# Performance work log

Measured on AMD Instinct MI355X. Metric: run time of the kernel, lower is better.

Reference implementation:

```python
import math
import jax, jax.numpy as jnp
import numpy as np

C = 128; NH = 8; NL = 4; NP = 4; DFF = 512; L = 3
RH, RW = 80, 240           # Rworld_shape
H, W = RH // 2, RW // 2    # per-level spatial shape after stride-2 downsample


def setup_inputs() -> dict:
    key = jax.random.key(0)
    ks = jax.random.split(key, 25)
    def n(k, shape, s=0.02):
        return jax.random.normal(k, shape, dtype=jnp.float32) * s
    return {
        "x": jax.random.normal(ks[0], (1, NL, C, RH, RW), dtype=jnp.float32),
        "dconv_w": n(ks[1], (C, C, 3, 3)),
        "dconv_b": n(ks[2], (C,)),
        "lvl_emb": n(ks[3], (NL, C), 1.0),
        "W_off": n(ks[4], (L, NH * NL * NP * 2, C)),
        "b_off": n(ks[5], (L, NH * NL * NP * 2), 0.1),
        "W_attn": n(ks[6], (L, NH * NL * NP, C)),
        "b_attn": n(ks[7], (L, NH * NL * NP)),
        "W_val": n(ks[8], (L, C, C)),
        "b_val": n(ks[9], (L, C)),
        "W_out": n(ks[10], (L, C, C)),
        "b_out": n(ks[11], (L, C)),
        "ln1_g": jnp.ones((L, C), jnp.float32),
        "ln1_b": jnp.zeros((L, C), jnp.float32),
        "W_ff1": n(ks[12], (L, DFF, C)),
        "b_ff1": n(ks[13], (L, DFF)),
        "W_ff2": n(ks[14], (L, C, DFF)),
        "b_ff2": n(ks[15], (L, C)),
        "ln2_g": jnp.ones((L, C), jnp.float32),
        "ln2_b": jnp.zeros((L, C), jnp.float32),
        "merge_w": n(ks[16], (C, C * NL, 1, 1)),
        "merge_b": n(ks[17], (C,)),
        "uconv_w": n(ks[18], (C, C, 3, 3)),
        "uconv_b": n(ks[19], (C,)),
    }


def conv2d(x, w, b, stride=1, pad=1):
    y = jax.lax.conv_general_dilated(x, w, (stride, stride), [(pad, pad), (pad, pad)],
                                     dimension_numbers=("NCHW", "OIHW", "NCHW"))
    return y + b[None, :, None, None]


def linear(x, w, b):
    return jnp.einsum("...i,oi->...o", x, w) + b


def layer_norm(x, g, b, eps=1e-5):
    m = jnp.mean(x, -1, keepdims=True)
    v = jnp.var(x, -1, keepdims=True)
    return (x - m) * jax.lax.rsqrt(v + eps) * g + b


def sine_pos_embed(h, w, nf, temperature=10000.0):
    # matches create_pos_embedding with normalize=True, scale=2*pi
    scale = 2.0 * math.pi
    eps = 1e-6
    ye = jnp.arange(1, h + 1, dtype=jnp.float32) / (h + eps) * scale
    xe = jnp.arange(1, w + 1, dtype=jnp.float32) / (w + eps) * scale
    i = jnp.arange(nf, dtype=jnp.float32)
    dim_t = temperature ** (2.0 * jnp.floor(i / 2.0) / nf)
    def enc(e):
        p = e[:, None] / dim_t
        return jnp.stack([jnp.sin(p[:, 0::2]), jnp.cos(p[:, 1::2])], -1).reshape(e.shape[0], nf)
    py, px = enc(ye), enc(xe)
    pos = jnp.concatenate([jnp.broadcast_to(py[:, None, :], (h, w, nf)),
                           jnp.broadcast_to(px[None, :, :], (h, w, nf))], -1)
    return pos  # (h, w, 2*nf) with [pos_y, pos_x] channel order


def ms_deform_attn_core(vmaps, loc, attn):
    # vmaps: (B,NL,NH,H*W,hd); loc: (B,Lq,NH,NL,NP,2) in [0,1] (x,y); attn: (B,Lq,NH,NL,NP)
    # grid_sample(align_corners=False, padding_mode='zeros') bilinear gather
    x = loc[..., 0] * W - 0.5
    y = loc[..., 1] * H - 0.5
    x0 = jnp.floor(x)
    y0 = jnp.floor(y)
    out = jnp.zeros((loc.shape[0], loc.shape[1], NH, vmaps.shape[-1]), loc.dtype)
    for dy in (0, 1):
        for dx in (0, 1):
            xc = x0 + dx
            yc = y0 + dy
            wgt = (1.0 - jnp.abs(x - xc)) * (1.0 - jnp.abs(y - yc))
            valid = (xc >= 0) & (xc < W) & (yc >= 0) & (yc < H)
            xi = jnp.clip(xc, 0, W - 1).astype(jnp.int32)
            yi = jnp.clip(yc, 0, H - 1).astype(jnp.int32)
            idx = (yi * W + xi).transpose(0, 3, 2, 1, 4)  # (B,NL,NH,Lq,NP)
            B_, nl, nh, lq, npt = idx.shape
            g = jnp.take_along_axis(vmaps, idx.reshape(B_, nl, nh, lq * npt, 1),
                                    axis=3).reshape(B_, nl, nh, lq, npt, -1)
            wv = (wgt * jnp.where(valid, 1.0, 0.0) * attn).transpose(0, 3, 2, 1, 4)
            out = out + jnp.einsum("blhqp,blhqpd->bqhd", wv, g)
    return out.reshape(out.shape[0], out.shape[1], -1)  # (B,Lq,NH*hd)


def reference(x, dconv_w, dconv_b, lvl_emb, W_off, b_off, W_attn, b_attn, W_val, b_val,
              W_out, b_out, ln1_g, ln1_b, W_ff1, b_ff1, W_ff2, b_ff2, ln2_g, ln2_b,
              merge_w, merge_b, uconv_w, uconv_b):
    B, N, c, h0, w0 = x.shape
    xs = jax.nn.relu(conv2d(x.reshape(B * N, c, h0, w0), dconv_w, dconv_b, stride=2))
    src = xs.reshape(B, N, c, H, W).transpose(0, 1, 3, 4, 2).reshape(B, N * H * W, c)
    pos = sine_pos_embed(H, W, c // 2).reshape(1, H * W, c) + lvl_emb[:, None, :]
    pos = pos.reshape(1, N * H * W, c)
    # reference points: per-level pixel centers (valid_ratios are all ones)
    ry = (jnp.arange(H, dtype=jnp.float32) + 0.5) / H
    rx = (jnp.arange(W, dtype=jnp.float32) + 0.5) / W
    ref = jnp.stack(jnp.meshgrid(rx, ry, indexing="xy"), -1).reshape(H * W, 2)
    ref = jnp.tile(ref, (N, 1))[None]  # (1, Lq, 2)
    hd = c // NH
    norm = jnp.array([W, H], jnp.float32)
    for i in range(W_off.shape[0]):
        q = src + pos
        value = linear(src, W_val[i], b_val[i]).reshape(B, N, H * W, NH, hd)
        vmaps = value.transpose(0, 1, 3, 2, 4)  # (B,NL,NH,HW,hd)
        off = linear(q, W_off[i], b_off[i]).reshape(B, -1, NH, N, NP, 2)
        aw = jax.nn.softmax(linear(q, W_attn[i], b_attn[i]).reshape(B, -1, NH, N * NP), -1)
        aw = aw.reshape(B, -1, NH, N, NP)
        loc = ref[:, :, None, None, None, :] + off / norm
        attn_out = ms_deform_attn_core(vmaps, loc, aw)
        src = layer_norm(src + linear(attn_out, W_out[i], b_out[i]), ln1_g[i], ln1_b[i])
        ff = linear(jax.nn.relu(linear(src, W_ff1[i], b_ff1[i])), W_ff2[i], b_ff2[i])
        src = layer_norm(src + ff, ln2_g[i], ln2_b[i])
    m = src.reshape(B, N, H, W, c).transpose(0, 1, 4, 2, 3).reshape(B, N * c, H, W)
    m = jax.nn.relu(conv2d(m, merge_w, merge_b, pad=0))
    m = jax.image.resize(m, (B, c, RH, RW), method="bilinear")
    m = jax.nn.relu(conv2d(m, uconv_w, uconv_b))
    return m
```

## Files before the change

kernel.cpp:

```cpp
#include <hip/hip_runtime.h>
#include <math.h>
#include <cstddef>

#define LQ   19200
#define HH   40
#define WW   120
#define HWp  4800
#define CCh  128
#define NHd  8
#define NLv  4
#define NPt  4
#define RHs  80
#define RWs  240

typedef __attribute__((ext_vector_type(8))) short bf16x8;
typedef __attribute__((ext_vector_type(4))) float f32x4;
typedef __attribute__((ext_vector_type(8))) _Float16 h16x8;
typedef __attribute__((address_space(1))) const unsigned int GUI;
typedef __attribute__((address_space(3))) unsigned int LUI;

__device__ inline unsigned short f2bf(float f) {
    unsigned int u = __float_as_uint(f);
    u += 0x7fffu + ((u >> 16) & 1u);
    return (unsigned short)(u >> 16);
}
__device__ inline float bf2f(unsigned int lo16) { return __uint_as_float(lo16 << 16); }

template<bool BIAS_ROW, bool RELU, int OMODE>
__global__ __launch_bounds__(256) void gemm_bf16(
    const unsigned short* __restrict__ A,
    const unsigned short* __restrict__ Bw,
    const float* __restrict__ bias,
    float* __restrict__ OutF, unsigned short* __restrict__ OutB,
    int M, int N, int K)
{
    constexpr int BM = 128, BN = 64, BK = 32;
    __shared__ unsigned short As[2][BM * BK];
    __shared__ unsigned short Bs[2][BN * BK];
    const int bm = blockIdx.y * BM, bn = blockIdx.x * BN;
    const int tid = threadIdx.x;
    const int wid = tid >> 6, lane = tid & 63;
    const int wm = (wid & 1) * 64, wn = (wid >> 1) * 32;
    const int lm = lane & 15, lqd = lane >> 4;

    f32x4 acc[4][2] = {};

    const int arow = lane >> 2;
    const int akc  = (lane & 3) * 8;
    const unsigned short* aG0 = A  + (size_t)(bm + wid * 32 +      arow) * K + akc;
    const unsigned short* aG1 = A  + (size_t)(bm + wid * 32 + 16 + arow) * K + akc;
    const unsigned short* bG  = Bw + (size_t)(bn + wid * 16 +      arow) * K + akc;
    const int aoff = wid * 1024 + lane * 8;
    const int boff = wid * 512 + lane * 8;

    auto stage = [&](int b, int k0) {
        __builtin_amdgcn_global_load_lds((GUI*)(aG0 + k0), (LUI*)(As[b] + aoff), 16, 0, 0);
        __builtin_amdgcn_global_load_lds((GUI*)(aG1 + k0), (LUI*)(As[b] + aoff + 512), 16, 0, 0);
        __builtin_amdgcn_global_load_lds((GUI*)(bG  + k0), (LUI*)(Bs[b] + boff), 16, 0, 0);
    };

    stage(0, 0);
    __syncthreads();
    int buf = 0;
    for (int k0 = 0; k0 < K; k0 += BK, buf ^= 1) {
        if (k0 + BK < K) stage(buf ^ 1, k0 + BK);
        bf16x8 a[4], b[2];
        #pragma unroll
        for (int i = 0; i < 4; i++)
            a[i] = *(const bf16x8*)(As[buf] + (wm + i * 16 + lm) * BK + lqd * 8);
        #pragma unroll
        for (int j = 0; j < 2; j++)
            b[j] = *(const bf16x8*)(Bs[buf] + (wn + j * 16 + lm) * BK + lqd * 8);
        #pragma unroll
        for (int i = 0; i < 4; i++)
            #pragma unroll
            for (int j = 0; j < 2; j++)
                acc[i][j] = __builtin_amdgcn_mfma_f32_16x16x32_bf16(a[i], b[j], acc[i][j], 0, 0, 0);
        __syncthreads();
    }

    #pragma unroll
    for (int i = 0; i < 4; i++) {
        int row0 = bm + wm + i * 16 + lqd * 4;
        #pragma unroll
        for (int j = 0; j < 2; j++) {
            int col = bn + wn + j * 16 + lm;
            float bc = BIAS_ROW ? 0.f : bias[col];
            #pragma unroll
            for (int r = 0; r < 4; r++) {
                int row = row0 + r;
                float v = acc[i][j][r] + (BIAS_ROW ? bias[row] : bc);
                if (RELU) v = fmaxf(v, 0.f);
                size_t o = (size_t)row * N + col;
                if (OMODE == 0) OutF[o] = v;
                else if (OMODE == 1) OutB[o] = f2bf(v);
                else { OutF[o] = v; OutB[o] = f2bf(v); }
            }
        }
    }
}

__global__ __launch_bounds__(256) void gemm_oav(
    const unsigned short* __restrict__ Aq,
    const unsigned short* __restrict__ Asrc,
    const unsigned short* __restrict__ Woa, const float* __restrict__ boa,
    const unsigned short* __restrict__ Wv,  const float* __restrict__ bv,
    _Float16* __restrict__ OutH, _Float16* __restrict__ OutH2,
    unsigned short* __restrict__ OutV)
{
    constexpr int BK = 32, K = 128;
    __shared__ unsigned short As[2][128 * BK];
    __shared__ unsigned short Bs[2][64 * BK];
    const int bx = blockIdx.x;
    const bool isv = bx >= 6;
    const unsigned short* A  = isv ? Asrc : Aq;
    const unsigned short* Bw = isv ? Wv : Woa;
    const float* bias = isv ? bv : boa;
    const int bn = isv ? (bx - 6) * 64 : bx * 64;
    const int bm = blockIdx.y * 128;
    const int tid = threadIdx.x;
    const int wid = tid >> 6, lane = tid & 63;
    const int wm = (wid & 1) * 64, wn = (wid >> 1) * 32;
    const int lm = lane & 15, lqd = lane >> 4;

    f32x4 acc[4][2] = {};

    const int arow = lane >> 2;
    const int akc  = (lane & 3) * 8;
    const unsigned short* aG0 = A  + (size_t)(bm + wid * 32 +      arow) * K + akc;
    const unsigned short* aG1 = A  + (size_t)(bm + wid * 32 + 16 + arow) * K + akc;
    const unsigned short* bG  = Bw + (size_t)(bn + wid * 16 +      arow) * K + akc;
    const int aoff = wid * 1024 + lane * 8;
    const int boff = wid * 512 + lane * 8;

    auto stage = [&](int b, int k0) {
        __builtin_amdgcn_global_load_lds((GUI*)(aG0 + k0), (LUI*)(As[b] + aoff), 16, 0, 0);
        __builtin_amdgcn_global_load_lds((GUI*)(aG1 + k0), (LUI*)(As[b] + aoff + 512), 16, 0, 0);
        __builtin_amdgcn_global_load_lds((GUI*)(bG  + k0), (LUI*)(Bs[b] + boff), 16, 0, 0);
    };

    stage(0, 0);
    __syncthreads();
    int buf = 0;
    for (int k0 = 0; k0 < K; k0 += BK, buf ^= 1) {
        if (k0 + BK < K) stage(buf ^ 1, k0 + BK);
        bf16x8 a[4], b[2];
        #pragma unroll
        for (int i = 0; i < 4; i++)
            a[i] = *(const bf16x8*)(As[buf] + (wm + i * 16 + lm) * BK + lqd * 8);
        #pragma unroll
        for (int j = 0; j < 2; j++)
            b[j] = *(const bf16x8*)(Bs[buf] + (wn + j * 16 + lm) * BK + lqd * 8);
        #pragma unroll
        for (int i = 0; i < 4; i++)
            #pragma unroll
            for (int j = 0; j < 2; j++)
                acc[i][j] = __builtin_amdgcn_mfma_f32_16x16x32_bf16(a[i], b[j], acc[i][j], 0, 0, 0);
        __syncthreads();
    }

    #pragma unroll
    for (int i = 0; i < 4; i++) {
        int row0 = bm + wm + i * 16 + lqd * 4;
        #pragma unroll
        for (int j = 0; j < 2; j++) {
            int col = bn + wn + j * 16 + lm;
            float bc = bias[col];
            if (!isv) {
                if (col < 256) {
                    #pragma unroll
                    for (int r = 0; r < 4; r++)
                        OutH[(size_t)(row0 + r) * 256 + col] = (_Float16)(acc[i][j][r] + bc);
                } else {
                    #pragma unroll
                    for (int r = 0; r < 4; r++) {
                        float v = acc[i][j][r] + bc;
                        float m = v;
                        #pragma unroll
                        for (int msk = 1; msk < 16; msk <<= 1)
                            m = fmaxf(m, __shfl_xor(m, msk));
                        float e = __expf(v - m);
                        float s = e;
                        #pragma unroll
                        for (int msk = 1; msk < 16; msk <<= 1)
                            s += __shfl_xor(s, msk);
                        OutH2[(size_t)(row0 + r) * 128 + (col - 256)] = (_Float16)(e / s);
                    }
                }
            } else {
                #pragma unroll
                for (int r = 0; r < 4; r++) {
                    int row = row0 + r;
                    int plane = (row / HWp) * 8 + (col >> 4);
                    size_t o = ((size_t)plane * HWp + (row % HWp)) * 16 + (col & 15);
                    OutV[o] = f2bf(acc[i][j][r] + bc);
                }
            }
        }
    }
}

template<bool WQ, bool WMERGE>
__global__ __launch_bounds__(256) void attn_ff(
    const unsigned short* __restrict__ attnout, const float* __restrict__ srcF_in,
    const unsigned short* __restrict__ Wout, const float* __restrict__ bout,
    const float* __restrict__ g1, const float* __restrict__ c1,
    const unsigned short* __restrict__ Wff1, const float* __restrict__ bff1,
    const unsigned short* __restrict__ Wff2, const float* __restrict__ bff2,
    const float* __restrict__ g2, const float* __restrict__ c2,
    float* __restrict__ outF, unsigned short* __restrict__ outB,
    const float* __restrict__ pos, unsigned short* __restrict__ qb,
    unsigned short* __restrict__ mergeb)
{
    __shared__ unsigned short fs[32 * 264];
    __shared__ unsigned short y1s[32 * 136];
    __shared__ float red[4][2][32];
    const int bm = blockIdx.x * 32;
    const int tid = threadIdx.x;
    const int wid = tid >> 6, lane = tid & 63;
    const int lm = lane & 15, lqd = lane >> 4;
    const int wn2 = wid * 32;

    float y1r[2][2][4];
    {
        f32x4 accA[2][2] = {};
        for (int k0 = 0; k0 < 128; k0 += 32) {
            int kc = k0 >> 5;
            bf16x8 a[2], b[2];
            #pragma unroll
            for (int i = 0; i < 2; i++)
                a[i] = *(const bf16x8*)(attnout + (size_t)(bm + i * 16 + lm) * 128 + k0 + lqd * 8);
            #pragma unroll
            for (int j = 0; j < 2; j++)
                b[j] = *(const bf16x8*)(Wout + ((size_t)((wid * 2 + j) * 4 + kc) * 64 + lane) * 8);
            #pragma unroll
            for (int i = 0; i < 2; i++)
                #pragma unroll
                for (int j = 0; j < 2; j++)
                    accA[i][j] = __builtin_amdgcn_mfma_f32_16x16x32_bf16(a[i], b[j], accA[i][j], 0, 0, 0);
        }
        #pragma unroll
        for (int i = 0; i < 2; i++)
            #pragma unroll
            for (int j = 0; j < 2; j++) {
                int col = wn2 + j * 16 + lm;
                float bc = bout[col];
                #pragma unroll
                for (int r = 0; r < 4; r++) {
                    int row = bm + i * 16 + lqd * 4 + r;
                    y1r[i][j][r] = accA[i][j][r] + bc + srcF_in[(size_t)row * 128 + col];
                }
            }
    }
    #pragma unroll
    for (int i = 0; i < 2; i++) {
        #pragma unroll
        for (int r = 0; r < 4; r++) {
            float s = y1r[i][0][r] + y1r[i][1][r];
            float q = y1r[i][0][r] * y1r[i][0][r] + y1r[i][1][r] * y1r[i][1][r];
            #pragma unroll
            for (int msk = 1; msk < 16; msk <<= 1) {
                s += __shfl_xor(s, msk);
                q += __shfl_xor(q, msk);
            }
            if (lm == 0) {
                int rl = i * 16 + lqd * 4 + r;
                red[wid][0][rl] = s;
                red[wid][1][rl] = q;
            }
        }
    }
    __syncthreads();
    #pragma unroll
    for (int i = 0; i < 2; i++) {
        float mean[4], inv[4];
        #pragma unroll
        for (int r = 0; r < 4; r++) {
            int rl = i * 16 + lqd * 4 + r;
            float s = red[0][0][rl] + red[1][0][rl] + red[2][0][rl] + red[3][0][rl];
            float q = red[0][1][rl] + red[1][1][rl] + red[2][1][rl] + red[3][1][rl];
            float m = s * (1.0f / 128.0f);
            float v = q * (1.0f / 128.0f) - m * m;
            mean[r] = m;
            inv[r] = rsqrtf(v + 1e-5f);
        }
        #pragma unroll
        for (int j = 0; j < 2; j++) {
            int col = wn2 + j * 16 + lm;
            float gc = g1[col], bc = c1[col];
            #pragma unroll
            for (int r = 0; r < 4; r++) {
                float y = (y1r[i][j][r] - mean[r]) * inv[r] * gc + bc;
                y1r[i][j][r] = y;
                y1s[(i * 16 + lqd * 4 + r) * 136 + col] = f2bf(y);
            }
        }
    }
    __syncthreads();

    f32x4 acc2[2][2] = {};
    for (int qc = 0; qc < 2; qc++) {
        {
            f32x4 accB[2][4] = {};
            for (int k0 = 0; k0 < 128; k0 += 32) {
                int kc = k0 >> 5;
                bf16x8 a[2], b[4];
                #pragma unroll
                for (int i = 0; i < 2; i++)
                    a[i] = *(const bf16x8*)(y1s + (i * 16 + lm) * 136 + k0 + lqd * 8);
                #pragma unroll
                for (int j = 0; j < 4; j++) {
                    int n0 = qc * 16 + wid * 4 + j;
                    b[j] = *(const bf16x8*)(Wff1 + ((size_t)(n0 * 4 + kc) * 64 + lane) * 8);
                }
                #pragma unroll
                for (int i = 0; i < 2; i++)
                    #pragma unroll
                    for (int j = 0; j < 4; j++)
                        accB[i][j] = __builtin_amdgcn_mfma_f32_16x16x32_bf16(a[i], b[j], accB[i][j], 0, 0, 0);
            }
            #pragma unroll
            for (int i = 0; i < 2; i++) {
                #pragma unroll
                for (int j = 0; j < 4; j++) {
                    int colc = wid * 64 + j * 16 + lm;
                    float bc = bff1[qc * 256 + colc];
                    #pragma unroll
                    for (int r = 0; r < 4; r++) {
                        int row = i * 16 + lqd * 4 + r;
                        fs[row * 264 + colc] = f2bf(fmaxf(accB[i][j][r] + bc, 0.f));
                    }
                }
            }
        }
        __syncthreads();
        for (int k0 = 0; k0 < 256; k0 += 32) {
            int kcg = qc * 8 + (k0 >> 5);
            bf16x8 a[2], b[2];
            #pragma unroll
            for (int i = 0; i < 2; i++)
                a[i] = *(const bf16x8*)(fs + (i * 16 + lm) * 264 + k0 + lqd * 8);
            #pragma unroll
            for (int j = 0; j < 2; j++)
                b[j] = *(const bf16x8*)(Wff2 + ((size_t)((wid * 2 + j) * 16 + kcg) * 64 + lane) * 8);
            #pragma unroll
            for (int i = 0; i < 2; i++)
                #pragma unroll
                for (int j = 0; j < 2; j++)
                    acc2[i][j] = __builtin_amdgcn_mfma_f32_16x16x32_bf16(a[i], b[j], acc2[i][j], 0, 0, 0);
        }
        __syncthreads();
    }

    float z[2][2][4];
    #pragma unroll
    for (int i = 0; i < 2; i++) {
        #pragma unroll
        for (int j = 0; j < 2; j++) {
            int col = wn2 + j * 16 + lm;
            float bc = bff2[col];
            #pragma unroll
            for (int r = 0; r < 4; r++)
                z[i][j][r] = acc2[i][j][r] + bc + y1r[i][j][r];
        }
    }
    #pragma unroll
    for (int i = 0; i < 2; i++) {
        #pragma unroll
        for (int r = 0; r < 4; r++) {
            float s = z[i][0][r] + z[i][1][r];
            float q = z[i][0][r] * z[i][0][r] + z[i][1][r] * z[i][1][r];
            #pragma unroll
            for (int msk = 1; msk < 16; msk <<= 1) {
                s += __shfl_xor(s, msk);
                q += __shfl_xor(q, msk);
            }
            if (lm == 0) {
                int rl = i * 16 + lqd * 4 + r;
                red[wid][0][rl] = s;
                red[wid][1][rl] = q;
            }
        }
    }
    __syncthreads();

    #pragma unroll
    for (int i = 0; i < 2; i++) {
        float mean[4], inv[4];
        #pragma unroll
        for (int r = 0; r < 4; r++) {
            int rl = i * 16 + lqd * 4 + r;
            float s = red[0][0][rl] + red[1][0][rl] + red[2][0][rl] + red[3][0][rl];
            float q = red[0][1][rl] + red[1][1][rl] + red[2][1][rl] + red[3][1][rl];
            float m = s * (1.0f / 128.0f);
            float v = q * (1.0f / 128.0f) - m * m;
            mean[r] = m;
            inv[r] = rsqrtf(v + 1e-5f);
        }
        #pragma unroll
        for (int j = 0; j < 2; j++) {
            int col = wn2 + j * 16 + lm;
            float gc = g2[col], bc2 = c2[col];
            #pragma unroll
            for (int r = 0; r < 4; r++) {
                int row = bm + i * 16 + lqd * 4 + r;
                float y = (z[i][j][r] - mean[r]) * inv[r] * gc + bc2;
                if constexpr (WMERGE) {
                    int n = row / HWp, pix = row % HWp;
                    mergeb[(size_t)pix * 512 + n * 128 + col] = f2bf(y);
                } else {
                    size_t o = (size_t)row * 128 + col;
                    outF[o] = y;
                    outB[o] = f2bf(y);
                    if constexpr (WQ) qb[o] = f2bf(y + pos[o]);
                }
            }
        }
    }
}

template<int MODE>
__global__ __launch_bounds__(256) void conv3x3_gemm(
    const unsigned short* __restrict__ X,
    const unsigned short* __restrict__ Wp,
    const float* __restrict__ bias,
    float* __restrict__ OutF, unsigned short* __restrict__ OutB,
    const float* __restrict__ pos, unsigned short* __restrict__ Qb)
{
    constexpr int BM = 64, BN = 64, BK = 32;
    constexpr int SMEM = (MODE == 1) ? 17408 : 16384;
    __shared__ __align__(16) unsigned char smem[SMEM];
    unsigned short* As = (unsigned short*)smem;
    unsigned short* Bs = (unsigned short*)(smem + 8192);
    const int bm = blockIdx.y * BM, bn = blockIdx.x * BN;
    const int tid = threadIdx.x;
    const int wid = tid >> 6, lane = tid & 63;
    const int wm = (wid & 1) * 32, wn = (wid >> 1) * 32;
    const int lm = lane & 15, lqd = lane >> 4;

    f32x4 acc[2][2] = {};

    const int arow = lane >> 2;
    const int akc  = (lane & 3) * 8;
    const int r0 = bm + wid * 16 + arow;
    size_t bA0;
    if (MODE == 0) {
        int n0 = r0 / HWp, rem0 = r0 % HWp, oh0 = rem0 / WW, ow0 = rem0 % WW;
        bA0 = ((size_t)(n0 * 82 + oh0 * 2) * 242 + ow0 * 2) * 128;
    } else {
        int y0 = r0 / RWs, x0 = r0 % RWs;
        bA0 = ((size_t)y0 * 242 + x0) * 128;
    }
    const unsigned short* bG = Wp + (size_t)(bn + wid * 16 + arow) * 1152 + akc;
    const int loff = wid * 512 + lane * 8;

    auto stage = [&](int b, int c) {
        int tap = c >> 2;
        int cpart = (c & 3) << 5;
        int ky = tap / 3, kx = tap % 3;
        int toff = (ky * 242 + kx) * 128 + cpart + akc;
        __builtin_amdgcn_global_load_lds((GUI*)(X + bA0 + toff), (LUI*)(As + b * 2048 + loff), 16, 0, 0);
        __builtin_amdgcn_global_load_lds((GUI*)(bG + c * 32), (LUI*)(Bs + b * 2048 + loff), 16, 0, 0);
    };

    stage(0, 0);
    __syncthreads();
    int buf = 0;
    for (int chunk = 0; chunk < 36; chunk++, buf ^= 1) {
        if (chunk < 35) stage(buf ^ 1, chunk + 1);
        bf16x8 a[2], b[2];
        #pragma unroll
        for (int i = 0; i < 2; i++)
            a[i] = *(const bf16x8*)(As + buf * 2048 + (wm + i * 16 + lm) * BK + lqd * 8);
        #pragma unroll
        for (int j = 0; j < 2; j++)
            b[j] = *(const bf16x8*)(Bs + buf * 2048 + (wn + j * 16 + lm) * BK + lqd * 8);
        #pragma unroll
        for (int i = 0; i < 2; i++)
            #pragma unroll
            for (int j = 0; j < 2; j++)
                acc[i][j] = __builtin_amdgcn_mfma_f32_16x16x32_bf16(a[i], b[j], acc[i][j], 0, 0, 0);
        __syncthreads();
    }

    if (MODE == 0) {
        #pragma unroll
        for (int i = 0; i < 2; i++) {
            int row0 = bm + wm + i * 16 + lqd * 4;
            #pragma unroll
            for (int j = 0; j < 2; j++) {
                int col = bn + wn + j * 16 + lm;
                float bc = bias[col];
                #pragma unroll
                for (int r = 0; r < 4; r++) {
                    float v = fmaxf(acc[i][j][r] + bc, 0.f);
                    size_t o = (size_t)(row0 + r) * 128 + col;
                    OutF[o] = v;
                    OutB[o] = f2bf(v);
                    Qb[o] = f2bf(v + pos[o]);
                }
            }
        }
    } else {
        float* Ts = (float*)smem;
        #pragma unroll
        for (int i = 0; i < 2; i++) {
            int lr0 = wm + i * 16 + lqd * 4;
            #pragma unroll
            for (int j = 0; j < 2; j++) {
                int lc = wn + j * 16 + lm;
                float bc = bias[bn + lc];
                #pragma unroll
                for (int r = 0; r < 4; r++)
                    Ts[lc * 68 + lr0 + r] = fmaxf(acc[i][j][r] + bc, 0.f);
            }
        }
        __syncthreads();
        for (int f = tid; f < 64 * 16; f += 256) {
            int ch = f >> 4, p4 = (f & 15) << 2;
            float4 v4 = *(const float4*)(Ts + ch * 68 + p4);
            *(float4*)(OutF + (size_t)(bn + ch) * 19200 + bm + p4) = v4;
        }
    }
}

__global__ __launch_bounds__(256) void prep_all(
    const float* __restrict__ W_val, const float* __restrict__ W_out,
    const float* __restrict__ W_ff1, const float* __restrict__ W_ff2,
    const float* __restrict__ merge_w,
    const float* __restrict__ Woff, const float* __restrict__ boff,
    const float* __restrict__ Wattn, const float* __restrict__ battn,
    const float* __restrict__ dconv_w, const float* __restrict__ uconv_w,
    const float* __restrict__ lvl_emb, const float* __restrict__ x,
    unsigned short* __restrict__ wb, unsigned short* __restrict__ wcat,
    float* __restrict__ bcat, unsigned short* __restrict__ dconv_wb,
    unsigned short* __restrict__ uconv_wb, unsigned short* __restrict__ xp,
    float* __restrict__ pos)
{
    __shared__ unsigned short t[240 * 36];
    int blk = blockIdx.x;
    if (blk >= 13831) {
        int b = blk - 13831;
        int ct = b & 3;
        int tmp = b >> 2;
        int y = tmp % 80, n = tmp / 80;
        const float* xin = x + (((size_t)(n * 128 + ct * 32)) * 80 + y) * 240;
        for (int f = threadIdx.x; f < 32 * 240; f += 256) {
            int c = f / 240, xc = f % 240;
            t[xc * 36 + c] = f2bf(xin[(size_t)c * 19200 + xc]);
        }
        __syncthreads();
        unsigned short* out = xp + (((size_t)(n * 82 + y + 1)) * 242 + 1) * 128 + ct * 32;
        for (int f = threadIdx.x; f < 240 * 8; f += 256) {
            int xc = f >> 3, c4 = (f & 7) << 2;
            ushort4 v = *(const ushort4*)(t + xc * 36 + c4);
            *(ushort4*)(out + (size_t)xc * 128 + c4) = v;
        }
        return;
    }
    int idx = blk * 256 + threadIdx.x;
    if (idx < 557056) {
        if (idx < 49152) {
            wb[idx] = f2bf(W_val[idx]);
        } else if (idx < 98304) {
            int rel = idx - 49152;
            int layer = rel >> 14, within = rel & 16383;
            int n = within >> 7, k = within & 127;
            int frag = ((((n >> 4) * 4 + (k >> 5)) * 4 + ((k >> 3) & 3)) * 16 + (n & 15)) * 8 + (k & 7);
            wb[49152 + (layer << 14) + frag] = f2bf(W_out[rel]);
        } else if (idx < 294912) {
            int rel = idx - 98304;
            int layer = rel >> 16, within = rel & 65535;
            int n = within >> 7, k = within & 127;
            int frag = ((((n >> 4) * 4 + (k >> 5)) * 4 + ((k >> 3) & 3)) * 16 + (n & 15)) * 8 + (k & 7);
            wb[98304 + (layer << 16) + frag] = f2bf(W_ff1[rel]);
        } else if (idx < 491520) {
            int rel = idx - 294912;
            int layer = rel >> 16, within = rel & 65535;
            int n = within >> 9, k = within & 511;
            int frag = ((((n >> 4) * 16 + (k >> 5)) * 4 + ((k >> 3) & 3)) * 16 + (n & 15)) * 8 + (k & 7);
            wb[294912 + (layer << 16) + frag] = f2bf(W_ff2[rel]);
        } else {
            wb[idx] = f2bf(merge_w[idx - 491520]);
        }
    } else if (idx < 705664) {
        int j = idx - 557056;
        if (j < 147456) {
            int layer = j / 49152, r = (j / 128) % 384, c = j & 127;
            float v = (r < 256) ? Woff[((size_t)layer * 256 + r) * 128 + c]
                                : Wattn[((size_t)layer * 128 + (r - 256)) * 128 + c];
            wcat[j] = f2bf(v);
        } else if (j < 148608) {
            int k = j - 147456;
            int layer = k / 384, r = k % 384;
            bcat[k] = (r < 256) ? boff[layer * 256 + r] : battn[layer * 128 + (r - 256)];
        }
    } else if (idx < 853120) {
        int j = idx - 705664;
        int cout = j / 1152, k = j % 1152;
        int tap = k >> 7, cin = k & 127;
        dconv_wb[j] = f2bf(dconv_w[(cout * 128 + cin) * 9 + tap]);
    } else if (idx < 1000576) {
        int j = idx - 853120;
        int cout = j / 1152, k = j % 1152;
        int tap = k >> 7, cin = k & 127;
        uconv_wb[j] = f2bf(uconv_w[(cout * 128 + cin) * 9 + tap]);
    } else if (idx < 1083008) {
        int j = idx - 1000576;
        int c4 = (j & 31) << 2;
        int tt = j >> 5;
        int p = tt % 644, n = tt / 644;
        int y, xx;
        if (p < 242)      { y = 0;       xx = p;       }
        else if (p < 484) { y = 81;      xx = p - 242; }
        else if (p < 564) { y = p - 483; xx = 0;       }
        else              { y = p - 563; xx = 241;     }
        ushort4 z = {0, 0, 0, 0};
        *(ushort4*)(xp + (((size_t)(n * 82 + y)) * 242 + xx) * 128 + c4) = z;
    } else if (idx < 3540608) {
        int j = idx - 1083008;
        int c = j & 127;
        int q = j >> 7;
        int n = q / HWp, pix = q % HWp;
        int h = pix / WW, w = pix % WW;
        int cc = (c < 64) ? c : (c - 64);
        float coord = (c < 64) ? (float)(h + 1) : (float)(w + 1);
        float denom = (c < 64) ? 40.0f : 120.0f;
        float e = coord / (denom + 1e-6f) * 6.283185307179586f;
        float expo = (float)(cc & ~1) * (1.0f / 64.0f);
        float dim_t = __expf(expo * 9.2103403719761836f);
        float p = e / dim_t;
        float v = (cc & 1) ? __cosf(p) : __sinf(p);
        pos[j] = v + lvl_emb[n * CCh + c];
    }
}

__device__ inline void fma8(float* acc, float w, uint4 v)
{
    acc[0] = fmaf(w, __uint_as_float(v.x << 16),          acc[0]);
    acc[1] = fmaf(w, __uint_as_float(v.x & 0xffff0000u),  acc[1]);
    acc[2] = fmaf(w, __uint_as_float(v.y << 16),          acc[2]);
    acc[3] = fmaf(w, __uint_as_float(v.y & 0xffff0000u),  acc[3]);
    acc[4] = fmaf(w, __uint_as_float(v.z << 16),          acc[4]);
    acc[5] = fmaf(w, __uint_as_float(v.z & 0xffff0000u),  acc[5]);
    acc[6] = fmaf(w, __uint_as_float(v.w << 16),          acc[6]);
    acc[7] = fmaf(w, __uint_as_float(v.w & 0xffff0000u),  acc[7]);
}
__device__ inline unsigned int pk2(float a, float b)
{ return (unsigned int)f2bf(a) | ((unsigned int)f2bf(b) << 16); }

__global__ __launch_bounds__(256) void deform_sample(
    const unsigned short* __restrict__ val, const _Float16* __restrict__ off,
    const _Float16* __restrict__ attn, unsigned short* __restrict__ out)
{
    int t = threadIdx.x;
    int bid = blockIdx.x;
    int h = bid & 7;
    int q = (bid >> 3) * 128 + (t >> 1);
    int half = t & 1;
    int pix = q % HWp;
    int qy = pix / WW, qx = pix % WW;
    const _Float16* offp = off + (size_t)q * 256 + h * 32;
    const _Float16* ap   = attn + (size_t)q * 128 + h * 16;
    h16x8 ovv[4];
    ovv[0] = *(const h16x8*)(offp);
    ovv[1] = *(const h16x8*)(offp + 8);
    ovv[2] = *(const h16x8*)(offp + 16);
    ovv[3] = *(const h16x8*)(offp + 24);
    h16x8 avv[2];
    avv[0] = *(const h16x8*)(ap);
    avv[1] = *(const h16x8*)(ap + 8);
    const unsigned short* vh = val + half * 8;
    float acc[8] = {};
    #pragma unroll
    for (int l = 0; l < 4; l++) {
        const unsigned short* vb = vh + (size_t)(l * 8 + h) * (HWp * 16);
        #pragma unroll
        for (int p = 0; p < 4; p++) {
            float ox = (float)ovv[l][2 * p];
            float oy = (float)ovv[l][2 * p + 1];
            int ai = l * 4 + p;
            float a = (float)avv[ai >> 3][ai & 7];
            float x = (float)qx + ox;
            float y = (float)qy + oy;
            float xf = floorf(x), yf = floorf(y);
            int x0 = (int)xf, y0 = (int)yf;
            float wx1 = x - xf, wy1 = y - yf;
            float wx0 = 1.f - wx1, wy0 = 1.f - wy1;
            #pragma unroll
            for (int dy = 0; dy < 2; dy++) {
                int yc = y0 + dy;
                bool vy = (unsigned)yc < (unsigned)HH;
                int yci = min(max(yc, 0), HH - 1);
                float wyv = dy ? wy1 : wy0;
                #pragma unroll
                for (int dx = 0; dx < 2; dx++) {
                    int xc = x0 + dx;
                    bool vld = vy && ((unsigned)xc < (unsigned)WW);
                    int xci = min(max(xc, 0), WW - 1);
                    float wgt = vld ? a * wyv * (dx ? wx1 : wx0) : 0.f;
                    uint4 v = *(const uint4*)(vb + (size_t)(yci * WW + xci) * 16);
                    fma8(acc, wgt, v);
                }
            }
        }
    }
    uint4 o = { pk2(acc[0], acc[1]), pk2(acc[2], acc[3]),
                pk2(acc[4], acc[5]), pk2(acc[6], acc[7]) };
    *(uint4*)(out + (size_t)q * CCh + h * 16 + half * 8) = o;
}

__global__ void upsample_nhwc(const float* __restrict__ m, unsigned short* __restrict__ up)
{
    unsigned idx = blockIdx.x * 256u + threadIdx.x;
    if (idx >= 82u * 242u * 32u) return;
    int c4 = (idx & 31) << 2;
    int p = idx >> 5;
    int px = p % 242, py = p / 242;
    ushort4 o = {0, 0, 0, 0};
    if (py >= 1 && py <= RHs && px >= 1 && px <= RWs) {
        int y = py - 1, x = px - 1;
        float fy = (y + 0.5f) * 0.5f - 0.5f;
        float fx = (x + 0.5f) * 0.5f - 0.5f;
        float fyf = floorf(fy), fxf = floorf(fx);
        int y0 = (int)fyf, x0 = (int)fxf;
        float wy = fy - fyf, wx = fx - fxf;
        int y0c = max(y0, 0), y1c = min(y0 + 1, HH - 1);
        int x0c = max(x0, 0), x1c = min(x0 + 1, WW - 1);
        unsigned short r[4];
        #pragma unroll
        for (int cc = 0; cc < 4; cc++) {
            const float* mp = m + (size_t)(c4 + cc) * HWp;
            float v00 = mp[y0c * WW + x0c], v01 = mp[y0c * WW + x1c];
            float v10 = mp[y1c * WW + x0c], v11 = mp[y1c * WW + x1c];
            float v = (1.f - wy) * ((1.f - wx) * v00 + wx * v01)
                    + wy * ((1.f - wx) * v10 + wx * v11);
            r[cc] = f2bf(v);
        }
        o.x = r[0]; o.y = r[1]; o.z = r[2]; o.w = r[3];
    }
    *(ushort4*)(up + (size_t)p * 128 + c4) = o;
}

extern "C" void kernel_launch(void* const* d_in, const int* in_sizes, int n_in,
                              void* d_out, int out_size, void* d_ws, size_t ws_size,
                              hipStream_t stream)
{
    const float* x       = (const float*)d_in[0];
    const float* dconv_w = (const float*)d_in[1];
    const float* dconv_b = (const float*)d_in[2];
    const float* lvl_emb = (const float*)d_in[3];
    const float* W_off   = (const float*)d_in[4];
    const float* b_off   = (const float*)d_in[5];
    const float* W_attn  = (const float*)d_in[6];
    const float* b_attn  = (const float*)d_in[7];
    const float* W_val   = (const float*)d_in[8];
    const float* b_val   = (const float*)d_in[9];
    const float* W_out   = (const float*)d_in[10];
    const float* b_out   = (const float*)d_in[11];
    const float* ln1_g   = (const float*)d_in[12];
    const float* ln1_b   = (const float*)d_in[13];
    const float* W_ff1   = (const float*)d_in[14];
    const float* b_ff1   = (const float*)d_in[15];
    const float* W_ff2   = (const float*)d_in[16];
    const float* b_ff2   = (const float*)d_in[17];
    const float* ln2_g   = (const float*)d_in[18];
    const float* ln2_b   = (const float*)d_in[19];
    const float* merge_w = (const float*)d_in[20];
    const float* merge_b = (const float*)d_in[21];
    const float* uconv_w = (const float*)d_in[22];
    const float* uconv_b = (const float*)d_in[23];

    char* wsb = (char*)d_ws;
    unsigned short* xp       = (unsigned short*)(wsb);
    unsigned short* up       = (unsigned short*)(wsb + 20320256);
    float*          src      = (float*)(wsb + 25400320);
    unsigned short* srcb     = (unsigned short*)(wsb + 35230720);
    float*          pos      = (float*)(wsb + 40145920);
    unsigned short* qb       = (unsigned short*)(wsb + 49976320);
    unsigned short* valb     = (unsigned short*)(wsb + 54891520);
    _Float16*       attnh    = (_Float16*)(wsb + 59806720);
    unsigned short* attnoutb = (unsigned short*)(wsb + 69637120);
    unsigned short* wb       = (unsigned short*)(wsb + 104043520);
    unsigned short* dconv_wb = (unsigned short*)(wsb + 105452544);
    unsigned short* uconv_wb = (unsigned short*)(wsb + 105747456);
    unsigned short* wcat     = (unsigned short*)(wsb + 106042368);
    float*          bcat     = (float*)(wsb + 106337280);
    _Float16*       offh     = (_Float16*)xp;
    unsigned short* merge_in = up;
    float*          mbuf     = (float*)valb;
    float* outp = (float*)d_out;

    unsigned short* W_val_b  = wb;
    unsigned short* W_out_b  = wb + 49152;
    unsigned short* W_ff1_b  = wb + 98304;
    unsigned short* W_ff2_b  = wb + 294912;
    unsigned short* merge_wb = wb + 491520;

    prep_all<<<15111, 256, 0, stream>>>(
        W_val, W_out, W_ff1, W_ff2, merge_w, W_off, b_off, W_attn, b_attn,
        dconv_w, uconv_w, lvl_emb, x,
        wb, wcat, bcat, dconv_wb, uconv_wb, xp, pos);

    conv3x3_gemm<0><<<dim3(2, 300), 256, 0, stream>>>(
        xp, dconv_wb, dconv_b, src, srcb, pos, qb);

    for (int i = 0; i < 3; i++) {
        gemm_oav<<<dim3(8, 150), 256, 0, stream>>>(
            qb, srcb,
            wcat + (size_t)i * 49152, bcat + i * 384,
            W_val_b + (size_t)i * 16384, b_val + i * 128,
            offh, attnh, valb);
        deform_sample<<<1200, 256, 0, stream>>>(valb, offh, attnh, attnoutb);
        if (i < 2) {
            attn_ff<true, false><<<600, 256, 0, stream>>>(
                attnoutb, src,
                W_out_b + (size_t)i * 16384, b_out + i * 128,
                ln1_g + i * 128, ln1_b + i * 128,
                W_ff1_b + (size_t)i * 65536, b_ff1 + i * 512,
                W_ff2_b + (size_t)i * 65536, b_ff2 + i * 128,
                ln2_g + i * 128, ln2_b + i * 128,
                src, srcb, pos, qb, nullptr);
        } else {
            attn_ff<false, true><<<600, 256, 0, stream>>>(
                attnoutb, src,
                W_out_b + (size_t)i * 16384, b_out + i * 128,
                ln1_g + i * 128, ln1_b + i * 128,
                W_ff1_b + (size_t)i * 65536, b_ff1 + i * 512,
                W_ff2_b + (size_t)i * 65536, b_ff2 + i * 128,
                ln2_g + i * 128, ln2_b + i * 128,
                nullptr, nullptr, nullptr, nullptr, merge_in);
        }
    }

    gemm_bf16<true, true, 0><<<dim3(75, 1), 256, 0, stream>>>(
        merge_wb, merge_in, merge_b, mbuf, nullptr, 128, 4800, 512);

    upsample_nhwc<<<2482, 256, 0, stream>>>(mbuf, up);

    conv3x3_gemm<1><<<dim3(2, 300), 256, 0, stream>>>(
        up, uconv_wb, uconv_b, outp, nullptr, nullptr, nullptr);
}
```

Before: 421.5 us.

## Factor positional embedding into row/col tables and widen oav GEMM tile to 128 columns

The full 19200x128 float positional-embedding buffer is replaced by two small sine tables (per row and per column) plus the level embedding, evaluated on the fly wherever q = src + pos is formed. This removes a large prep write and the repeated pos reads in the conv and attn_ff epilogues, at the cost of some integer div/mod per element. Separately, the fused offset/attention/value GEMM now uses 128-wide N tiles (4 column blocks instead of 8), so each A tile is loaded half as often, but each wave holds twice the accumulators.

```diff
diff --git a/kernel.cpp b/kernel.cpp
--- a/kernel.cpp
+++ b/kernel.cpp
@@ -26,6 +26,17 @@
 }
 __device__ inline float bf2f(unsigned int lo16) { return __uint_as_float(lo16 << 16); }
 
+__device__ inline float pos_eval(const float* __restrict__ ty,
+                                 const float* __restrict__ tx,
+                                 const float* __restrict__ lvl,
+                                 int row, int col)
+{
+    int n = row / HWp, pix = row % HWp;
+    int hh = pix / WW, wx = pix % WW;
+    float t = (col < 64) ? ty[hh * 64 + col] : tx[wx * 64 + (col - 64)];
+    return t + lvl[n * CCh + col];
+}
+
 template<bool BIAS_ROW, bool RELU, int OMODE>
 __global__ __launch_bounds__(256) void gemm_bf16(
     const unsigned short* __restrict__ A,
@@ -110,33 +121,34 @@
 {
     constexpr int BK = 32, K = 128;
     __shared__ unsigned short As[2][128 * BK];
-    __shared__ unsigned short Bs[2][64 * BK];
+    __shared__ unsigned short Bs[2][128 * BK];
     const int bx = blockIdx.x;
-    const bool isv = bx >= 6;
+    const bool isv = bx == 3;
     const unsigned short* A  = isv ? Asrc : Aq;
     const unsigned short* Bw = isv ? Wv : Woa;
     const float* bias = isv ? bv : boa;
-    const int bn = isv ? (bx - 6) * 64 : bx * 64;
+    const int bn = isv ? 0 : bx * 128;
     const int bm = blockIdx.y * 128;
     const int tid = threadIdx.x;
     const int wid = tid >> 6, lane = tid & 63;
-    const int wm = (wid & 1) * 64, wn = (wid >> 1) * 32;
+    const int wm = (wid & 1) * 64, wn = (wid >> 1) * 64;
     const int lm = lane & 15, lqd = lane >> 4;
 
-    f32x4 acc[4][2] = {};
+    f32x4 acc[4][4] = {};
 
     const int arow = lane >> 2;
     const int akc  = (lane & 3) * 8;
     const unsigned short* aG0 = A  + (size_t)(bm + wid * 32 +      arow) * K + akc;
     const unsigned short* aG1 = A  + (size_t)(bm + wid * 32 + 16 + arow) * K + akc;
-    const unsigned short* bG  = Bw + (size_t)(bn + wid * 16 +      arow) * K + akc;
-    const int aoff = wid * 1024 + lane * 8;
-    const int boff = wid * 512 + lane * 8;
+    const unsigned short* bG0 = Bw + (size_t)(bn + wid * 32 +      arow) * K + akc;
+    const unsigned short* bG1 = Bw + (size_t)(bn + wid * 32 + 16 + arow) * K + akc;
+    const int loff = wid * 1024 + lane * 8;
 
     auto stage = [&](int b, int k0) {
-        __builtin_amdgcn_global_load_lds((GUI*)(aG0 + k0), (LUI*)(As[b] + aoff), 16, 0, 0);
-        __builtin_amdgcn_global_load_lds((GUI*)(aG1 + k0), (LUI*)(As[b] + aoff + 512), 16, 0, 0);
-        __builtin_amdgcn_global_load_lds((GUI*)(bG  + k0), (LUI*)(Bs[b] + boff), 16, 0, 0);
+        __builtin_amdgcn_global_load_lds((GUI*)(aG0 + k0), (LUI*)(As[b] + loff), 16, 0, 0);
+        __builtin_amdgcn_global_load_lds((GUI*)(aG1 + k0), (LUI*)(As[b] + loff + 512), 16, 0, 0);
+        __builtin_amdgcn_global_load_lds((GUI*)(bG0 + k0), (LUI*)(Bs[b] + loff), 16, 0, 0);
+        __builtin_amdgcn_global_load_lds((GUI*)(bG1 + k0), (LUI*)(Bs[b] + loff + 512), 16, 0, 0);
     };
 
     stage(0, 0);
@@ -144,17 +156,17 @@
     int buf = 0;
     for (int k0 = 0; k0 < K; k0 += BK, buf ^= 1) {
         if (k0 + BK < K) stage(buf ^ 1, k0 + BK);
-        bf16x8 a[4], b[2];
+        bf16x8 a[4], b[4];
         #pragma unroll
         for (int i = 0; i < 4; i++)
             a[i] = *(const bf16x8*)(As[buf] + (wm + i * 16 + lm) * BK + lqd * 8);
         #pragma unroll
-        for (int j = 0; j < 2; j++)
+        for (int j = 0; j < 4; j++)
             b[j] = *(const bf16x8*)(Bs[buf] + (wn + j * 16 + lm) * BK + lqd * 8);
         #pragma unroll
         for (int i = 0; i < 4; i++)
             #pragma unroll
-            for (int j = 0; j < 2; j++)
+            for (int j = 0; j < 4; j++)
                 acc[i][j] = __builtin_amdgcn_mfma_f32_16x16x32_bf16(a[i], b[j], acc[i][j], 0, 0, 0);
         __syncthreads();
     }
@@ -163,8 +175,9 @@
     for (int i = 0; i < 4; i++) {
         int row0 = bm + wm + i * 16 + lqd * 4;
         #pragma unroll
-        for (int j = 0; j < 2; j++) {
-            int col = bn + wn + j * 16 + lm;
+        for (int j = 0; j < 4; j++) {
+            int coll = wn + j * 16 + lm;
+            int col  = bn + coll;
             float bc = bias[col];
             if (!isv) {
                 if (col < 256) {
@@ -191,8 +204,8 @@
                 #pragma unroll
                 for (int r = 0; r < 4; r++) {
                     int row = row0 + r;
-                    int plane = (row / HWp) * 8 + (col >> 4);
-                    size_t o = ((size_t)plane * HWp + (row % HWp)) * 16 + (col & 15);
+                    int plane = (row / HWp) * 8 + (coll >> 4);
+                    size_t o = ((size_t)plane * HWp + (row % HWp)) * 16 + (coll & 15);
                     OutV[o] = f2bf(acc[i][j][r] + bc);
                 }
             }
@@ -209,7 +222,8 @@
     const unsigned short* __restrict__ Wff2, const float* __restrict__ bff2,
     const float* __restrict__ g2, const float* __restrict__ c2,
     float* __restrict__ outF, unsigned short* __restrict__ outB,
-    const float* __restrict__ pos, unsigned short* __restrict__ qb,
+    const float* __restrict__ ty, const float* __restrict__ tx,
+    const float* __restrict__ lvl, unsigned short* __restrict__ qb,
     unsigned short* __restrict__ mergeb)
 {
     __shared__ unsigned short fs[32 * 264];
@@ -412,7 +426,8 @@
                     size_t o = (size_t)row * 128 + col;
                     outF[o] = y;
                     outB[o] = f2bf(y);
-                    if constexpr (WQ) qb[o] = f2bf(y + pos[o]);
+                    if constexpr (WQ)
+                        qb[o] = f2bf(y + pos_eval(ty, tx, lvl, row, col));
                 }
             }
         }
@@ -425,7 +440,8 @@
     const unsigned short* __restrict__ Wp,
     const float* __restrict__ bias,
     float* __restrict__ OutF, unsigned short* __restrict__ OutB,
-    const float* __restrict__ pos, unsigned short* __restrict__ Qb)
+    const float* __restrict__ ty, const float* __restrict__ tx,
+    const float* __restrict__ lvl, unsigned short* __restrict__ Qb)
 {
     constexpr int BM = 64, BN = 64, BK = 32;
     constexpr int SMEM = (MODE == 1) ? 17408 : 16384;
@@ -493,11 +509,12 @@
                 float bc = bias[col];
                 #pragma unroll
                 for (int r = 0; r < 4; r++) {
+                    int row = row0 + r;
                     float v = fmaxf(acc[i][j][r] + bc, 0.f);
-                    size_t o = (size_t)(row0 + r) * 128 + col;
+                    size_t o = (size_t)row * 128 + col;
                     OutF[o] = v;
                     OutB[o] = f2bf(v);
-                    Qb[o] = f2bf(v + pos[o]);
+                    Qb[o] = f2bf(v + pos_eval(ty, tx, lvl, row, col));
                 }
             }
         }
@@ -531,16 +548,16 @@
     const float* __restrict__ Woff, const float* __restrict__ boff,
     const float* __restrict__ Wattn, const float* __restrict__ battn,
     const float* __restrict__ dconv_w, const float* __restrict__ uconv_w,
-    const float* __restrict__ lvl_emb, const float* __restrict__ x,
+    const float* __restrict__ x,
     unsigned short* __restrict__ wb, unsigned short* __restrict__ wcat,
     float* __restrict__ bcat, unsigned short* __restrict__ dconv_wb,
     unsigned short* __restrict__ uconv_wb, unsigned short* __restrict__ xp,
-    float* __restrict__ pos)
+    float* __restrict__ ty, float* __restrict__ tx)
 {
     __shared__ unsigned short t[240 * 36];
     int blk = blockIdx.x;
-    if (blk >= 13831) {
-        int b = blk - 13831;
+    if (blk >= 4271) {
+        int b = blk - 4271;
         int ct = b & 3;
         int tmp = b >> 2;
         int y = tmp % 80, n = tmp / 80;
@@ -617,21 +634,23 @@
         else              { y = p - 563; xx = 241;     }
         ushort4 z = {0, 0, 0, 0};
         *(ushort4*)(xp + (((size_t)(n * 82 + y)) * 242 + xx) * 128 + c4) = z;
-    } else if (idx < 3540608) {
+    } else if (idx < 1093248) {
         int j = idx - 1083008;
-        int c = j & 127;
-        int q = j >> 7;
-        int n = q / HWp, pix = q % HWp;
-        int h = pix / WW, w = pix % WW;
-        int cc = (c < 64) ? c : (c - 64);
-        float coord = (c < 64) ? (float)(h + 1) : (float)(w + 1);
-        float denom = (c < 64) ? 40.0f : 120.0f;
-        float e = coord / (denom + 1e-6f) * 6.283185307179586f;
+        int cc = j & 63;
         float expo = (float)(cc & ~1) * (1.0f / 64.0f);
         float dim_t = __expf(expo * 9.2103403719761836f);
-        float p = e / dim_t;
-        float v = (cc & 1) ? __cosf(p) : __sinf(p);
-        pos[j] = v + lvl_emb[n * CCh + c];
+        if (j < 2560) {
+            int hh = j >> 6;
+            float e = (float)(hh + 1) / (40.0f + 1e-6f) * 6.283185307179586f;
+            float p = e / dim_t;
+            ty[j] = (cc & 1) ? __cosf(p) : __sinf(p);
+        } else {
+            int j2 = j - 2560;
+            int wx = j2 >> 6;
+            float e = (float)(wx + 1) / (120.0f + 1e-6f) * 6.283185307179586f;
+            float p = e / dim_t;
+            tx[j2] = (cc & 1) ? __cosf(p) : __sinf(p);
+        }
     }
 }
 
@@ -776,7 +795,8 @@
     unsigned short* up       = (unsigned short*)(wsb + 20320256);
     float*          src      = (float*)(wsb + 25400320);
     unsigned short* srcb     = (unsigned short*)(wsb + 35230720);
-    float*          pos      = (float*)(wsb + 40145920);
+    float*          ty       = (float*)(wsb + 40145920);
+    float*          tx       = (float*)(wsb + 40156160);
     unsigned short* qb       = (unsigned short*)(wsb + 49976320);
     unsigned short* valb     = (unsigned short*)(wsb + 54891520);
     _Float16*       attnh    = (_Float16*)(wsb + 59806720);
@@ -797,16 +817,16 @@
     unsigned short* W_ff2_b  = wb + 294912;
     unsigned short* merge_wb = wb + 491520;
 
-    prep_all<<<15111, 256, 0, stream>>>(
+    prep_all<<<5551, 256, 0, stream>>>(
         W_val, W_out, W_ff1, W_ff2, merge_w, W_off, b_off, W_attn, b_attn,
-        dconv_w, uconv_w, lvl_emb, x,
-        wb, wcat, bcat, dconv_wb, uconv_wb, xp, pos);
+        dconv_w, uconv_w, x,
+        wb, wcat, bcat, dconv_wb, uconv_wb, xp, ty, tx);
 
     conv3x3_gemm<0><<<dim3(2, 300), 256, 0, stream>>>(
-        xp, dconv_wb, dconv_b, src, srcb, pos, qb);
+        xp, dconv_wb, dconv_b, src, srcb, ty, tx, lvl_emb, qb);
 
     for (int i = 0; i < 3; i++) {
-        gemm_oav<<<dim3(8, 150), 256, 0, stream>>>(
+        gemm_oav<<<dim3(4, 150), 256, 0, stream>>>(
             qb, srcb,
             wcat + (size_t)i * 49152, bcat + i * 384,
             W_val_b + (size_t)i * 16384, b_val + i * 128,
@@ -820,7 +840,7 @@
                 W_ff1_b + (size_t)i * 65536, b_ff1 + i * 512,
                 W_ff2_b + (size_t)i * 65536, b_ff2 + i * 128,
                 ln2_g + i * 128, ln2_b + i * 128,
-                src, srcb, pos, qb, nullptr);
+                src, srcb, ty, tx, lvl_emb, qb, nullptr);
         } else {
             attn_ff<false, true><<<600, 256, 0, stream>>>(
                 attnoutb, src,
@@ -829,7 +849,7 @@
                 W_ff1_b + (size_t)i * 65536, b_ff1 + i * 512,
                 W_ff2_b + (size_t)i * 65536, b_ff2 + i * 128,
                 ln2_g + i * 128, ln2_b + i * 128,
-                nullptr, nullptr, nullptr, nullptr, merge_in);
+                nullptr, nullptr, nullptr, nullptr, nullptr, nullptr, merge_in);
         }
     }
 
@@ -839,5 +859,5 @@
     upsample_nhwc<<<2482, 256, 0, stream>>>(mbuf, up);
 
     conv3x3_gemm<1><<<dim3(2, 300), 256, 0, stream>>>(
-        up, uconv_wb, uconv_b, outp, nullptr, nullptr, nullptr);
-}
+        up, uconv_wb, uconv_b, outp, nullptr, nullptr, nullptr, nullptr, nullptr);
+}
```

Result: slower. 468.3 us (+11.1%).
